# Kernel optimization log

Hardware: AMD Instinct MI355X
Metric: run time of the kernel (lower is better)

## Reference

```python
import jax, jax.numpy as jnp
import numpy as np
import math

N, T, D, H = 2, 4096, 768, 12
DH = D // H


def setup_inputs() -> dict:
    key = jax.random.key(0)
    ks = jax.random.split(key, 6)
    x = jax.random.normal(ks[0], (N, T, D), dtype=jnp.float32)
    # key-padding mask: True = masked out; mask the last quarter of positions
    mask = jnp.broadcast_to(jnp.arange(T) >= (3 * T) // 4, (N, T))
    scale = 0.02
    Wq = jax.random.normal(ks[1], (D, D), dtype=jnp.float32) * scale
    Wk = jax.random.normal(ks[2], (D, D), dtype=jnp.float32) * scale
    Wv = jax.random.normal(ks[3], (D, D), dtype=jnp.float32) * scale
    Wo = jax.random.normal(ks[4], (D, D), dtype=jnp.float32) * scale
    zb = jnp.zeros((D,), dtype=jnp.float32)
    return {"x": x, "mask": mask, "Wq": Wq, "bq": zb, "Wk": Wk, "bk": zb,
            "Wv": Wv, "bv": zb, "Wo": Wo, "bo": zb}


def reference(x, mask, Wq, bq, Wk, bk, Wv, bv, Wo, bo):
    n, t, d = x.shape
    h, dh = H, d // H
    # torch Linear: y = x @ W.T + b
    def proj(W, b):
        return (x @ W.T + b).reshape(n, t, h, dh).transpose(0, 2, 1, 3)  # [n,h,t,dh]
    q = proj(Wq, bq)
    k = proj(Wk, bk)
    v = proj(Wv, bv)
    s = jnp.einsum('nhqd,nhkd->nhqk', q, k) / math.sqrt(dh)  # [n,h,t,t]
    s = jnp.where(mask[:, None, None, :], -jnp.inf, s)
    p = jax.nn.softmax(s, axis=-1)
    # dropout prob 0.0 / eval mode -> identity
    a = jnp.einsum('nhqk,nhkd->nhqd', p, v)  # [n,h,t,dh]
    a = a.transpose(0, 2, 1, 3).reshape(n, t, d)
    return a @ Wo.T + bo
```

## Files before the change

kernel.cpp:

```cpp
#include <hip/hip_runtime.h>
#include <hip/hip_bf16.h>
#include <stdint.h>

#define T_SEQ 4096
#define DM    768
#define NHEAD 12
#define DHEAD 64
#define NBAT  2
#define LOG2E 1.4426950408889634f

typedef __bf16 bf16x8 __attribute__((ext_vector_type(8)));
typedef float  f32x4  __attribute__((ext_vector_type(4)));

static __device__ __forceinline__ unsigned short f2bf(float f) {
  unsigned int u = __builtin_bit_cast(unsigned int, f);
  u += 0x7FFFu + ((u >> 16) & 1u);
  return (unsigned short)(u >> 16);
}
static __device__ __forceinline__ unsigned short f2bf_hw(float f) {
  __hip_bfloat16 h = __float2bfloat16(f);
  return __builtin_bit_cast(unsigned short, h);
}
static __device__ __forceinline__ unsigned int pk2(float lo, float hi) {
  return (unsigned int)f2bf_hw(lo) | ((unsigned int)f2bf_hw(hi) << 16);
}
static __device__ __forceinline__ void gll16(const void* g, void* l) {
  __builtin_amdgcn_global_load_lds(
      (const __attribute__((address_space(1))) unsigned int*)g,
      (__attribute__((address_space(3))) unsigned int*)l, 16, 0, 0);
}
static __device__ __forceinline__ bf16x8 ldfrag(const unsigned short* p) {
  const unsigned short* q = (const unsigned short*)__builtin_assume_aligned(p, 16);
  bf16x8 v;
  __builtin_memcpy(&v, q, 16);
  return v;
}
static __device__ __forceinline__ void st8(unsigned short* p, uint2 v) {
  __builtin_memcpy(__builtin_assume_aligned(p, 8), &v, 8);
}
static __device__ __forceinline__ uint2 ld8(const unsigned short* p) {
  uint2 v;
  __builtin_memcpy(&v, __builtin_assume_aligned(p, 8), 8);
  return v;
}

__global__ void cvt_kernel(const float* __restrict__ s, unsigned short* __restrict__ d, int n) {
  int i = (blockIdx.x * 256 + threadIdx.x) * 4;
  if (i < n) {
    float4 v = *(const float4*)(s + i);
    ushort4 o;
    o.x = f2bf(v.x); o.y = f2bf(v.y); o.z = f2bf(v.z); o.w = f2bf(v.w);
    *(ushort4*)(d + i) = o;
  }
}
__global__ void cvt4_kernel(const float* __restrict__ s0, const float* __restrict__ s1,
                            const float* __restrict__ s2, const float* __restrict__ s3,
                            unsigned short* __restrict__ d0, unsigned short* __restrict__ d1,
                            unsigned short* __restrict__ d2, unsigned short* __restrict__ d3,
                            int n) {
  int w = blockIdx.y;
  const float* sp = (w == 0) ? s0 : (w == 1) ? s1 : (w == 2) ? s2 : s3;
  unsigned short* dp = (w == 0) ? d0 : (w == 1) ? d1 : (w == 2) ? d2 : d3;
  int i = (blockIdx.x * 256 + threadIdx.x) * 4;
  if (i < n) {
    float4 v = *(const float4*)(sp + i);
    ushort4 o;
    o.x = f2bf(v.x); o.y = f2bf(v.y); o.z = f2bf(v.z); o.w = f2bf(v.w);
    *(ushort4*)(dp + i) = o;
  }
}

__global__ void init_kernel(int* __restrict__ kmx) {
  if (threadIdx.x < NBAT) { kmx[threadIdx.x] = 0; kmx[NBAT + threadIdx.x] = T_SEQ; }
}

__global__ void build_bias_kernel(const unsigned char* __restrict__ mraw,
                                  float* __restrict__ bias,
                                  int* __restrict__ kmx) {
  int idx = blockIdx.x * 256 + threadIdx.x;
  int is_u8 = (mraw[(3 * T_SEQ) / 4] != 0);
  int masked;
  if (is_u8) masked = (mraw[idx] != 0);
  else       masked = (((const int*)mraw)[idx] != 0);
  bias[idx] = masked ? -1e9f : 0.0f;
  __shared__ int smax, smin;
  if (threadIdx.x == 0) { smax = 0; smin = T_SEQ; }
  __syncthreads();
  int pos = idx & (T_SEQ - 1);
  if (!masked) atomicMax(&smax, pos + 1);
  else         atomicMin(&smin, pos);
  __syncthreads();
  if (threadIdx.x == 0) {
    atomicMax(&kmx[idx >> 12], smax);
    atomicMin(&kmx[NBAT + (idx >> 12)], smin);
  }
}

template <int MODE>
__global__ __launch_bounds__(256, 2) void gemm128(
    const unsigned short* __restrict__ A,
    const unsigned short* __restrict__ W0, const unsigned short* __restrict__ W1,
    const unsigned short* __restrict__ W2,
    const float* __restrict__ Bb0, const float* __restrict__ Bb1,
    const float* __restrict__ Bb2,
    void* __restrict__ O0, void* __restrict__ O1, void* __restrict__ O2) {
  constexpr int NT = (MODE == 0) ? 8 : 4;
  constexpr int NROWS = NT * 32;
  __shared__ __align__(16) unsigned short lA[128 * 64];
  __shared__ __align__(16) unsigned short lB[NROWS * 64];
  const int t = threadIdx.x;
  const int lane = t & 63, quad = lane >> 4, l16 = lane & 15;
  const int wave = t >> 6;
  const int moff = (wave & 1) * 64, noff = (wave >> 1) * (NT * 16);
  const int m0 = blockIdx.x * 128;
  const int by = blockIdx.y;
  const unsigned short* W;
  const float* Bb;
  int o0, wsel = 0;
  if constexpr (MODE == 0) {
    wsel = by / 3;
    o0 = (by % 3) * 256;
    W  = (wsel == 0) ? W0  : ((wsel == 1) ? W1  : W2);
    Bb = (wsel == 0) ? Bb0 : ((wsel == 1) ? Bb1 : Bb2);
  } else {
    o0 = by * 128; W = W0; Bb = Bb0;
  }
  f32x4 acc[4][NT];
#pragma unroll
  for (int i = 0; i < 4; ++i)
#pragma unroll
    for (int j = 0; j < NT; ++j) acc[i][j] = (f32x4){0.f, 0.f, 0.f, 0.f};

  for (int k0 = 0; k0 < DM; k0 += 64) {
#pragma unroll
    for (int i = 0; i < 4; ++i) {
      int c = i * 256 + t;
      int r = c >> 3;
      int qc = (c & 7) ^ (r & 7);
      gll16(A + (size_t)(m0 + r) * DM + k0 + qc * 8, &lA[(i * 256 + (t & 192)) * 8]);
    }
#pragma unroll
    for (int i = 0; i < NT; ++i) {
      int c = i * 256 + t;
      int r = c >> 3;
      int qc = (c & 7) ^ (r & 7);
      gll16(W + (size_t)(o0 + r) * DM + k0 + qc * 8, &lB[(i * 256 + (t & 192)) * 8]);
    }
    __syncthreads();
    bf16x8 af[4][2];
#pragma unroll
    for (int mt = 0; mt < 4; ++mt) {
      int r = moff + mt * 16 + l16;
#pragma unroll
      for (int s = 0; s < 2; ++s)
        af[mt][s] = ldfrag(&lA[(r * 8 + ((s * 4 + quad) ^ (r & 7))) * 8]);
    }
#pragma unroll
    for (int nt = 0; nt < NT; ++nt) {
      int r = noff + nt * 16 + l16;
      bf16x8 b0 = ldfrag(&lB[(r * 8 + ((quad) ^ (r & 7))) * 8]);
      bf16x8 b1 = ldfrag(&lB[(r * 8 + ((4 + quad) ^ (r & 7))) * 8]);
#pragma unroll
      for (int mt = 0; mt < 4; ++mt) {
        acc[mt][nt] = __builtin_amdgcn_mfma_f32_16x16x32_bf16(af[mt][0], b0, acc[mt][nt], 0, 0, 0);
        acc[mt][nt] = __builtin_amdgcn_mfma_f32_16x16x32_bf16(af[mt][1], b1, acc[mt][nt], 0, 0, 0);
      }
    }
    __syncthreads();
  }
#pragma unroll
  for (int nt = 0; nt < NT; ++nt) {
    int o = o0 + noff + nt * 16 + l16;
    float bias = Bb[o];
    if (MODE == 0 && wsel == 2) {
      int h = o >> 6, d = o & 63;
#pragma unroll
      for (int mt = 0; mt < 4; ++mt) {
        int m = m0 + moff + mt * 16 + quad * 4;
        int n = m >> 12, tb = m & (T_SEQ - 1);
        uint2 w;
        w.x = pk2(acc[mt][nt][0] + bias, acc[mt][nt][1] + bias);
        w.y = pk2(acc[mt][nt][2] + bias, acc[mt][nt][3] + bias);
        *(uint2*)((unsigned short*)O2 +
                  ((size_t)(n * NHEAD + h) * DHEAD + d) * T_SEQ + tb) = w;
      }
      continue;
    }
#pragma unroll
    for (int mt = 0; mt < 4; ++mt) {
#pragma unroll
      for (int r = 0; r < 4; ++r) {
        int m = m0 + moff + mt * 16 + quad * 4 + r;
        float v = acc[mt][nt][r] + bias;
        if constexpr (MODE == 0) {
          int n = m >> 12, tt = m & (T_SEQ - 1);
          int h = o >> 6, d = o & 63;
          if (wsel == 0)
            ((unsigned short*)O0)[((size_t)(n * NHEAD + h) * T_SEQ + tt) * DHEAD + d] = f2bf(v * (0.125f * LOG2E));
          else
            ((unsigned short*)O1)[((size_t)(n * NHEAD + h) * T_SEQ + tt) * DHEAD + d] = f2bf(v);
        } else {
          ((float*)O0)[(size_t)m * DM + o] = v;
        }
      }
    }
  }
}

__global__ __launch_bounds__(256, 3) void flash_kernel(
    const unsigned short* __restrict__ Q, const unsigned short* __restrict__ K,
    const unsigned short* __restrict__ VT, const float* __restrict__ bias,
    const int* __restrict__ kmx, unsigned short* __restrict__ Aout) {
  __shared__ __align__(16) unsigned short lK[128 * 64];
  __shared__ __align__(16) unsigned short lV[64 * 128];
  const int t = threadIdx.x;
  const int lane = t & 63, quad = lane >> 4, l16 = lane & 15;
  const int wave = t >> 6;
  const int nh = blockIdx.y;
  const int n = nh / NHEAD, h = nh % NHEAD;
  const int q0 = blockIdx.x * 128;
  const size_t base = (size_t)nh * T_SEQ * DHEAD;

  bf16x8 qf[2][2];
#pragma unroll
  for (int qt = 0; qt < 2; ++qt) {
    int qrow = q0 + wave * 32 + qt * 16 + l16;
    qf[qt][0] = ldfrag(Q + base + (size_t)qrow * DHEAD + quad * 8);
    qf[qt][1] = ldfrag(Q + base + (size_t)qrow * DHEAD + 32 + quad * 8);
  }

  bf16x8 vone;
#pragma unroll
  for (int i = 0; i < 8; ++i) vone[i] = (__bf16)1.0f;

  f32x4 oacc[2][4], oaccl[2];
#pragma unroll
  for (int qt = 0; qt < 2; ++qt) {
#pragma unroll
    for (int dt = 0; dt < 4; ++dt) oacc[qt][dt] = (f32x4){0.f, 0.f, 0.f, 0.f};
    oaccl[qt] = (f32x4){0.f, 0.f, 0.f, 0.f};
  }

  const int km = kmx[n], fm = kmx[NBAT + n];
  int ntiles = (km + 127) >> 7;
  if (ntiles > (T_SEQ >> 7)) ntiles = T_SEQ >> 7;
  const float* brow = bias + (size_t)n * T_SEQ;

  const int idxA = ((((quad & 1) << 1) * 16) + l16) << 2;
  const int idxB = idxA + 64;
  const bool hiq = (quad >= 2);

  for (int it = 0; it < ntiles; ++it) {
    const int j0 = it << 7;
#pragma unroll
    for (int i = 0; i < 4; ++i) {
      int c = i * 256 + t;
      int r = c >> 3;
      int qc = (c & 7) ^ (r & 7);
      gll16(K + base + (size_t)(j0 + r) * DHEAD + qc * 8, &lK[(i * 256 + (t & 192)) * 8]);
    }
#pragma unroll
    for (int i = 0; i < 4; ++i) {
      int c = i * 256 + t;
      int r = c >> 4;
      int qc = (c & 15) ^ (r & 15);
      gll16(VT + base + (size_t)r * T_SEQ + j0 + qc * 8, &lV[(i * 256 + (t & 192)) * 8]);
    }
    __syncthreads();

    f32x4 sacc[2][8];
#pragma unroll
    for (int qt = 0; qt < 2; ++qt)
#pragma unroll
      for (int nt = 0; nt < 8; ++nt) sacc[qt][nt] = (f32x4){0.f, 0.f, 0.f, 0.f};
#pragma unroll
    for (int nt = 0; nt < 8; ++nt) {
      int r = nt * 16 + l16;
      bf16x8 k0f = ldfrag(&lK[(r * 8 + (quad ^ (r & 7))) * 8]);
      bf16x8 k1f = ldfrag(&lK[(r * 8 + ((4 + quad) ^ (r & 7))) * 8]);
#pragma unroll
      for (int qt = 0; qt < 2; ++qt) {
        sacc[qt][nt] = __builtin_amdgcn_mfma_f32_16x16x32_bf16(k0f, qf[qt][0], sacc[qt][nt], 0, 0, 0);
        sacc[qt][nt] = __builtin_amdgcn_mfma_f32_16x16x32_bf16(k1f, qf[qt][1], sacc[qt][nt], 0, 0, 0);
      }
    }
    if (j0 + 128 > fm) {
#pragma unroll
      for (int nt = 0; nt < 8; ++nt) {
        float4 bv = *(const float4*)&brow[j0 + nt * 16 + quad * 4];
#pragma unroll
        for (int qt = 0; qt < 2; ++qt) {
          sacc[qt][nt][0] += bv.x; sacc[qt][nt][1] += bv.y;
          sacc[qt][nt][2] += bv.z; sacc[qt][nt][3] += bv.w;
        }
      }
    }
    unsigned int pd[2][8][2];
#pragma unroll
    for (int qt = 0; qt < 2; ++qt)
#pragma unroll
      for (int nt = 0; nt < 8; ++nt) {
        pd[qt][nt][0] = pk2(__builtin_exp2f(sacc[qt][nt][0]), __builtin_exp2f(sacc[qt][nt][1]));
        pd[qt][nt][1] = pk2(__builtin_exp2f(sacc[qt][nt][2]), __builtin_exp2f(sacc[qt][nt][3]));
      }
#pragma unroll
    for (int kb = 0; kb < 4; ++kb) {
      bf16x8 pb[2];
#pragma unroll
      for (int qt = 0; qt < 2; ++qt) {
        unsigned int t0, t1;
        uint4 bw;
        t0 = (unsigned int)__builtin_amdgcn_ds_bpermute(idxA, (int)pd[qt][2 * kb][0]);
        t1 = (unsigned int)__builtin_amdgcn_ds_bpermute(idxA, (int)pd[qt][2 * kb + 1][0]);
        bw.x = hiq ? t1 : t0;
        t0 = (unsigned int)__builtin_amdgcn_ds_bpermute(idxA, (int)pd[qt][2 * kb][1]);
        t1 = (unsigned int)__builtin_amdgcn_ds_bpermute(idxA, (int)pd[qt][2 * kb + 1][1]);
        bw.y = hiq ? t1 : t0;
        t0 = (unsigned int)__builtin_amdgcn_ds_bpermute(idxB, (int)pd[qt][2 * kb][0]);
        t1 = (unsigned int)__builtin_amdgcn_ds_bpermute(idxB, (int)pd[qt][2 * kb + 1][0]);
        bw.z = hiq ? t1 : t0;
        t0 = (unsigned int)__builtin_amdgcn_ds_bpermute(idxB, (int)pd[qt][2 * kb][1]);
        t1 = (unsigned int)__builtin_amdgcn_ds_bpermute(idxB, (int)pd[qt][2 * kb + 1][1]);
        bw.w = hiq ? t1 : t0;
        pb[qt] = __builtin_bit_cast(bf16x8, bw);
      }
#pragma unroll
      for (int dt = 0; dt < 4; ++dt) {
        int rv = dt * 16 + l16;
        bf16x8 vf = ldfrag(&lV[(rv * 16 + ((kb * 4 + quad) ^ (rv & 15))) * 8]);
#pragma unroll
        for (int qt = 0; qt < 2; ++qt)
          oacc[qt][dt] = __builtin_amdgcn_mfma_f32_16x16x32_bf16(vf, pb[qt], oacc[qt][dt], 0, 0, 0);
      }
#pragma unroll
      for (int qt = 0; qt < 2; ++qt)
        oaccl[qt] = __builtin_amdgcn_mfma_f32_16x16x32_bf16(vone, pb[qt], oaccl[qt], 0, 0, 0);
    }
    __syncthreads();
  }
  unsigned short* lO = &lK[wave * (32 * 68)];
#pragma unroll
  for (int qt = 0; qt < 2; ++qt) {
    float l = oaccl[qt][0];
    float rl = (l > 0.f) ? 1.0f / l : 0.f;
#pragma unroll
    for (int dt = 0; dt < 4; ++dt) {
      uint2 w;
      w.x = pk2(oacc[qt][dt][0] * rl, oacc[qt][dt][1] * rl);
      w.y = pk2(oacc[qt][dt][2] * rl, oacc[qt][dt][3] * rl);
      st8(lO + (qt * 16 + l16) * 68 + dt * 16 + quad * 4, w);
    }
  }
#pragma unroll
  for (int it2 = 0; it2 < 8; ++it2) {
    int rowq = it2 * 4 + quad;
    uint2 w = ld8(lO + rowq * 68 + l16 * 4);
    int tt = q0 + wave * 32 + rowq;
    *(uint2*)(Aout + (size_t)(n * T_SEQ + tt) * DM + h * DHEAD + l16 * 4) = w;
  }
}

extern "C" void kernel_launch(void* const* d_in, const int* in_sizes, int n_in,
                              void* d_out, int out_size, void* d_ws, size_t ws_size,
                              hipStream_t stream) {
  const float*         x  = (const float*)d_in[0];
  const unsigned char* mk = (const unsigned char*)d_in[1];
  const float* Wq = (const float*)d_in[2];
  const float* bq = (const float*)d_in[3];
  const float* Wk = (const float*)d_in[4];
  const float* bk = (const float*)d_in[5];
  const float* Wv = (const float*)d_in[6];
  const float* bv = (const float*)d_in[7];
  const float* Wo = (const float*)d_in[8];
  const float* bo = (const float*)d_in[9];

  const int xe = NBAT * T_SEQ * DM;
  const int we = DM * DM;
  const size_t xb_bytes = (size_t)xe * 2;
  const size_t wb_bytes = (size_t)we * 2;
  const size_t kv_bytes = (size_t)NBAT * NHEAD * T_SEQ * DHEAD * 2;

  auto rnd = [](size_t b) { return (b + 255) & ~(size_t)255; };
  size_t need = rnd(xb_bytes) + 4 * rnd(wb_bytes) + 2 * rnd(kv_bytes) +
                rnd((size_t)NBAT * T_SEQ * 4) + 256;
  if (ws_size < need) return;

  char* ws = (char*)d_ws;
  size_t off = 0;
  auto alloc = [&](size_t b) { char* p = ws + off; off += rnd(b); return p; };
  unsigned short* x_b  = (unsigned short*)alloc(xb_bytes);
  unsigned short* wq_b = (unsigned short*)alloc(wb_bytes);
  unsigned short* wk_b = (unsigned short*)alloc(wb_bytes);
  unsigned short* wv_b = (unsigned short*)alloc(wb_bytes);
  unsigned short* wo_b = (unsigned short*)alloc(wb_bytes);
  unsigned short* k_ws  = (unsigned short*)alloc(kv_bytes);
  unsigned short* vt_ws = (unsigned short*)alloc(kv_bytes);
  float* bias = (float*)alloc((size_t)NBAT * T_SEQ * 4);
  int* kmx    = (int*)alloc(256);
  unsigned short* q_ws = (unsigned short*)d_out;
  unsigned short* a_ws = x_b;

  init_kernel<<<1, 64, 0, stream>>>(kmx);
  cvt_kernel<<<xe / 1024, 256, 0, stream>>>(x, x_b, xe);
  cvt4_kernel<<<dim3(we / 1024, 4), 256, 0, stream>>>(
      Wq, Wk, Wv, Wo, wq_b, wk_b, wv_b, wo_b, we);
  build_bias_kernel<<<(NBAT * T_SEQ) / 256, 256, 0, stream>>>(mk, bias, kmx);
  gemm128<0><<<dim3((NBAT * T_SEQ) / 128, 9), 256, 0, stream>>>(
      x_b, wq_b, wk_b, wv_b, bq, bk, bv, q_ws, k_ws, vt_ws);
  flash_kernel<<<dim3(T_SEQ / 128, NBAT * NHEAD), 256, 0, stream>>>(
      q_ws, k_ws, vt_ws, bias, kmx, a_ws);
  gemm128<1><<<dim3((NBAT * T_SEQ) / 128, DM / 128), 256, 0, stream>>>(
      a_ws, wo_b, wo_b, wo_b, bo, bo, bo, d_out, d_out, d_out);
  (void)in_sizes; (void)n_in; (void)out_size;
}
```

Measured before the change: 316.1 us.

## Double-buffer K/V tiles in flash kernel, remap blocks, and retile GEMMs

The flash attention kernel now double-buffers K and V tiles in LDS, issuing the next tile's global-to-LDS loads before computing on the current one. This hides load latency and removes one barrier per iteration. Its launch becomes a 1D grid with a block-to-(head, query tile) mapping meant to spread heads across CUs and improve K/V cache locality. Because of the doubled LDS, its occupancy target drops from 3 to 2 blocks. Both GEMMs use narrower N tiles (192 and 96 instead of 256 and 128) with more blocks, giving better wave balance, and the QKV GEMM targets 3 blocks per CU.

```diff
diff --git a/kernel.cpp b/kernel.cpp
--- a/kernel.cpp
+++ b/kernel.cpp
@@ -97,14 +97,14 @@
 }
 
 template <int MODE>
-__global__ __launch_bounds__(256, 2) void gemm128(
+__global__ __launch_bounds__(256, (MODE == 0) ? 3 : 2) void gemm128(
     const unsigned short* __restrict__ A,
     const unsigned short* __restrict__ W0, const unsigned short* __restrict__ W1,
     const unsigned short* __restrict__ W2,
     const float* __restrict__ Bb0, const float* __restrict__ Bb1,
     const float* __restrict__ Bb2,
     void* __restrict__ O0, void* __restrict__ O1, void* __restrict__ O2) {
-  constexpr int NT = (MODE == 0) ? 8 : 4;
+  constexpr int NT = (MODE == 0) ? 6 : 3;
   constexpr int NROWS = NT * 32;
   __shared__ __align__(16) unsigned short lA[128 * 64];
   __shared__ __align__(16) unsigned short lB[NROWS * 64];
@@ -118,12 +118,12 @@
   const float* Bb;
   int o0, wsel = 0;
   if constexpr (MODE == 0) {
-    wsel = by / 3;
-    o0 = (by % 3) * 256;
+    wsel = by >> 2;
+    o0 = (by & 3) * 192;
     W  = (wsel == 0) ? W0  : ((wsel == 1) ? W1  : W2);
     Bb = (wsel == 0) ? Bb0 : ((wsel == 1) ? Bb1 : Bb2);
   } else {
-    o0 = by * 128; W = W0; Bb = Bb0;
+    o0 = by * 96; W = W0; Bb = Bb0;
   }
   f32x4 acc[4][NT];
 #pragma unroll
@@ -207,18 +207,20 @@
   }
 }
 
-__global__ __launch_bounds__(256, 3) void flash_kernel(
+__global__ __launch_bounds__(256, 2) void flash_kernel(
     const unsigned short* __restrict__ Q, const unsigned short* __restrict__ K,
     const unsigned short* __restrict__ VT, const float* __restrict__ bias,
     const int* __restrict__ kmx, unsigned short* __restrict__ Aout) {
-  __shared__ __align__(16) unsigned short lK[128 * 64];
-  __shared__ __align__(16) unsigned short lV[64 * 128];
+  __shared__ __align__(16) unsigned short lK[2][128 * 64];
+  __shared__ __align__(16) unsigned short lV[2][64 * 128];
   const int t = threadIdx.x;
   const int lane = t & 63, quad = lane >> 4, l16 = lane & 15;
   const int wave = t >> 6;
-  const int nh = blockIdx.y;
-  const int n = nh / NHEAD, h = nh % NHEAD;
-  const int q0 = blockIdx.x * 128;
+  const int b = blockIdx.x;
+  const int slot = b >> 3;
+  const int nh = (b & 7) * 3 + (slot % 3);
+  const int q0 = (slot / 3) * 128;
+  const int n = nh / NHEAD, h = nh - n * NHEAD;
   const size_t base = (size_t)nh * T_SEQ * DHEAD;
 
   bf16x8 qf[2][2];
@@ -250,23 +252,32 @@
   const int idxB = idxA + 64;
   const bool hiq = (quad >= 2);
 
-  for (int it = 0; it < ntiles; ++it) {
-    const int j0 = it << 7;
+  auto stage = [&](int j0, int buf) {
 #pragma unroll
     for (int i = 0; i < 4; ++i) {
       int c = i * 256 + t;
       int r = c >> 3;
       int qc = (c & 7) ^ (r & 7);
-      gll16(K + base + (size_t)(j0 + r) * DHEAD + qc * 8, &lK[(i * 256 + (t & 192)) * 8]);
+      gll16(K + base + (size_t)(j0 + r) * DHEAD + qc * 8,
+            &lK[buf][(i * 256 + (t & 192)) * 8]);
     }
 #pragma unroll
     for (int i = 0; i < 4; ++i) {
       int c = i * 256 + t;
       int r = c >> 4;
       int qc = (c & 15) ^ (r & 15);
-      gll16(VT + base + (size_t)r * T_SEQ + j0 + qc * 8, &lV[(i * 256 + (t & 192)) * 8]);
-    }
+      gll16(VT + base + (size_t)r * T_SEQ + j0 + qc * 8,
+            &lV[buf][(i * 256 + (t & 192)) * 8]);
+    }
+  };
+
+  stage(0, 0);
+
+  for (int it = 0; it < ntiles; ++it) {
+    const int j0 = it << 7;
+    const int buf = it & 1;
     __syncthreads();
+    if (it + 1 < ntiles) stage((it + 1) << 7, buf ^ 1);
 
     f32x4 sacc[2][8];
 #pragma unroll
@@ -276,8 +287,8 @@
 #pragma unroll
     for (int nt = 0; nt < 8; ++nt) {
       int r = nt * 16 + l16;
-      bf16x8 k0f = ldfrag(&lK[(r * 8 + (quad ^ (r & 7))) * 8]);
-      bf16x8 k1f = ldfrag(&lK[(r * 8 + ((4 + quad) ^ (r & 7))) * 8]);
+      bf16x8 k0f = ldfrag(&lK[buf][(r * 8 + (quad ^ (r & 7))) * 8]);
+      bf16x8 k1f = ldfrag(&lK[buf][(r * 8 + ((4 + quad) ^ (r & 7))) * 8]);
 #pragma unroll
       for (int qt = 0; qt < 2; ++qt) {
         sacc[qt][nt] = __builtin_amdgcn_mfma_f32_16x16x32_bf16(k0f, qf[qt][0], sacc[qt][nt], 0, 0, 0);
@@ -327,7 +338,7 @@
 #pragma unroll
       for (int dt = 0; dt < 4; ++dt) {
         int rv = dt * 16 + l16;
-        bf16x8 vf = ldfrag(&lV[(rv * 16 + ((kb * 4 + quad) ^ (rv & 15))) * 8]);
+        bf16x8 vf = ldfrag(&lV[buf][(rv * 16 + ((kb * 4 + quad) ^ (rv & 15))) * 8]);
 #pragma unroll
         for (int qt = 0; qt < 2; ++qt)
           oacc[qt][dt] = __builtin_amdgcn_mfma_f32_16x16x32_bf16(vf, pb[qt], oacc[qt][dt], 0, 0, 0);
@@ -336,9 +347,9 @@
       for (int qt = 0; qt < 2; ++qt)
         oaccl[qt] = __builtin_amdgcn_mfma_f32_16x16x32_bf16(vone, pb[qt], oaccl[qt], 0, 0, 0);
     }
-    __syncthreads();
-  }
-  unsigned short* lO = &lK[wave * (32 * 68)];
+  }
+  __syncthreads();
+  unsigned short* lO = &lK[0][wave * (32 * 68)];
 #pragma unroll
   for (int qt = 0; qt < 2; ++qt) {
     float l = oaccl[qt][0];
@@ -405,11 +416,11 @@
   cvt4_kernel<<<dim3(we / 1024, 4), 256, 0, stream>>>(
       Wq, Wk, Wv, Wo, wq_b, wk_b, wv_b, wo_b, we);
   build_bias_kernel<<<(NBAT * T_SEQ) / 256, 256, 0, stream>>>(mk, bias, kmx);
-  gemm128<0><<<dim3((NBAT * T_SEQ) / 128, 9), 256, 0, stream>>>(
+  gemm128<0><<<dim3((NBAT * T_SEQ) / 128, 12), 256, 0, stream>>>(
       x_b, wq_b, wk_b, wv_b, bq, bk, bv, q_ws, k_ws, vt_ws);
-  flash_kernel<<<dim3(T_SEQ / 128, NBAT * NHEAD), 256, 0, stream>>>(
+  flash_kernel<<<NBAT * NHEAD * (T_SEQ / 128), 256, 0, stream>>>(
       q_ws, k_ws, vt_ws, bias, kmx, a_ws);
-  gemm128<1><<<dim3((NBAT * T_SEQ) / 128, DM / 128), 256, 0, stream>>>(
+  gemm128<1><<<dim3((NBAT * T_SEQ) / 128, 8), 256, 0, stream>>>(
       a_ws, wo_b, wo_b, wo_b, bo, bo, bo, d_out, d_out, d_out);
   (void)in_sizes; (void)n_in; (void)out_size;
 }
```

Result: slower. 326.1 us (+3.2%).
